# Optimization experiments

Measured on AMD Instinct MI355X. Metric: run time of the kernel, lower is better.

## Reference

```python
import jax, jax.numpy as jnp
import numpy as np

C = 128      # block channels
K = 7        # involution kernel size
GC = 16      # group_ch
G = (C // 2) // GC  # involution groups = 4


def conv1x1(x, w, b):
    # x: (B,Cin,H,W), w: (Cout,Cin)
    return jnp.einsum('bchw,oc->bohw', x, w) + b[None, :, None, None]


def conv2d(x, w, b, pad):
    y = jax.lax.conv_general_dilated(
        x, w, window_strides=(1, 1), padding=((pad, pad), (pad, pad)),
        dimension_numbers=('NCHW', 'OIHW', 'NCHW'))
    return y + b[None, :, None, None]


def prelu(x, a):
    return jnp.where(x >= 0, x, a * x)


def patches7(x):
    # x: (B,C,H,W) -> (B,C,K*K,H,W), same padding (torch Unfold, pad=3)
    B, Cc, H, W = x.shape
    p = K // 2
    xp = jnp.pad(x, ((0, 0), (0, 0), (p, p), (p, p)))
    return jnp.stack([xp[:, :, i:i + H, j:j + W]
                      for i in range(K) for j in range(K)], axis=2)


def setup_inputs() -> dict:
    key = jax.random.key(0)
    ks = jax.random.split(key, 9)
    f32 = jnp.float32
    def w(k, shape, s=0.02):
        return jax.random.normal(k, shape, f32) * s
    d = {}
    d['x'] = jax.random.normal(ks[0], (2, C, 128, 128), f32)
    # conv1: C -> C//2, 1x1
    d['w1'] = w(ks[1], (C // 2, C)); d['b1'] = jnp.zeros((C // 2,), f32)
    d['a1'] = jnp.float32(0.25)  # PReLU (single param)
    # involution reduce: C//2 -> C//4, 1x1 (+ReLU)
    d['wr'] = w(ks[2], (C // 4, C // 2)); d['br'] = jnp.zeros((C // 4,), f32)
    # involution span: C//4 -> G*K*K, 1x1
    d['ws'] = w(ks[3], (G * K * K, C // 4)); d['bs'] = jnp.zeros((G * K * K,), f32)
    d['a2'] = jnp.float32(0.25)
    # conv2: C//2 -> C, 1x1
    d['w2'] = w(ks[4], (C, C // 2)); d['b2'] = jnp.zeros((C,), f32)
    # attn conv: 2 -> 1, 7x7 pad 3
    d['wa'] = w(ks[5], (1, 2, 7, 7)); d['ba'] = jnp.zeros((1,), f32)
    # psec: 3x3 (C//4->C//4) + PReLU + 1x1 (C//4->C)
    d['wp1'] = w(ks[6], (C // 4, C // 4, 3, 3)); d['bp1'] = jnp.zeros((C // 4,), f32)
    d['ap'] = jnp.float32(0.25)
    d['wp2'] = w(ks[7], (C, C // 4)); d['bp2'] = jnp.zeros((C,), f32)
    return d


def reference(x, w1, b1, a1, wr, br, ws, bs, a2, w2, b2, wa, ba, wp1, bp1, ap, wp2, bp2):
    B, _, H, W = x.shape
    x1 = prelu(conv1x1(x, w1, b1), a1)                       # (B, C/2, H, W)
    # involution: per-pixel dynamic kernels
    f = jax.nn.relu(conv1x1(x1, wr, br))                     # (B, C/4, H, W)
    kw = conv1x1(f, ws, bs).reshape(B, G, 1, K * K, H, W)    # dynamic kernels
    pat = patches7(x1).reshape(B, G, GC, K * K, H, W)        # unfolded patches
    x2 = (kw * pat).sum(axis=3).reshape(B, C // 2, H, W)     # multiply-reduce
    x3 = conv1x1(prelu(x2, a2), w2, b2)                      # (B, C, H, W)
    # attention gate on f (ZPool -> 7x7 conv -> sigmoid)
    zp = jnp.concatenate([f.max(axis=1, keepdims=True),
                          f.mean(axis=1, keepdims=True)], axis=1)
    attn = jax.nn.sigmoid(conv2d(zp, wa, ba, 3))             # (B, 1, H, W)
    x4 = x3 * attn
    ps = conv1x1(prelu(conv2d(f, wp1, bp1, 1), ap), wp2, bp2)
    return x4 + ps
```

## Files before the change

### kernel.cpp

```cpp
#include <hip/hip_runtime.h>

#define HW_  16384
#define NPX  32768

__device__ __forceinline__ float prelu_(float x, float a) { return x >= 0.f ? x : a * x; }

__global__ __launch_bounds__(256, 2) void k_front(const float* __restrict__ x,
        const float* __restrict__ w1, const float* __restrict__ b1,
        const float* __restrict__ a1p, const float* __restrict__ wr,
        const float* __restrict__ br, float* __restrict__ x1,
        float* __restrict__ f, float* __restrict__ zp) {
    __shared__ float sA[12352];
    float* xs  = sA;
    float* wT1 = sA + 4096;
    int p0 = blockIdx.x << 6;
    int b = p0 >> 14, hw0 = p0 & 16383;

    for (int e = threadIdx.x; e < 8192; e += 256) {
        int o = e >> 7, c = e & 127;
        wT1[o * 129 + c] = w1[e];
    }
    int pq = threadIdx.x & 15;
    int og = threadIdx.x >> 4;
    const float a1 = a1p[0];
    float4 acc[4];
    #pragma unroll
    for (int u = 0; u < 4; ++u) { float bv = b1[og * 4 + u]; acc[u] = make_float4(bv, bv, bv, bv); }
    const float* xb = x + (b << 21) + hw0;
    #pragma unroll 1
    for (int half = 0; half < 2; ++half) {
        float4 xv[4];
        #pragma unroll
        for (int i = 0; i < 4; ++i) {
            int e = threadIdx.x + (i << 8);
            xv[i] = *(const float4*)&xb[((half * 64 + (e >> 4)) << 14) + ((e & 15) << 2)];
        }
        __syncthreads();
        #pragma unroll
        for (int i = 0; i < 4; ++i) {
            int e = threadIdx.x + (i << 8);
            *(float4*)&xs[((e >> 4) << 6) + ((e & 15) << 2)] = xv[i];
        }
        __syncthreads();
        #pragma unroll 4
        for (int c2 = 0; c2 < 64; ++c2) {
            float4 tap = *(const float4*)&xs[(c2 << 6) + (pq << 2)];
            int c = (half << 6) + c2;
            #pragma unroll
            for (int u = 0; u < 4; ++u) {
                float wv = wT1[(og * 4 + u) * 129 + c];
                acc[u].x = fmaf(wv, tap.x, acc[u].x);
                acc[u].y = fmaf(wv, tap.y, acc[u].y);
                acc[u].z = fmaf(wv, tap.z, acc[u].z);
                acc[u].w = fmaf(wv, tap.w, acc[u].w);
            }
        }
    }
    float4 res[4];
    #pragma unroll
    for (int u = 0; u < 4; ++u) {
        res[u].x = prelu_(acc[u].x, a1); res[u].y = prelu_(acc[u].y, a1);
        res[u].z = prelu_(acc[u].z, a1); res[u].w = prelu_(acc[u].w, a1);
        *(float4*)(x1 + ((b * 64 + og * 4 + u) << 14) + hw0 + (pq << 2)) = res[u];
    }
    __syncthreads();
    float* x1t = sA;
    float* wrT = sA + 4352;
    float* ft  = sA + 6432;
    #pragma unroll
    for (int u = 0; u < 4; ++u)
        *(float4*)&x1t[(og * 4 + u) * 68 + (pq << 2)] = res[u];
    for (int e = threadIdx.x; e < 2048; e += 256) {
        int fo = e >> 6, c = e & 63;
        wrT[fo * 65 + c] = wr[e];
    }
    __syncthreads();
    int pq2 = threadIdx.x & 15;
    int fg = threadIdx.x >> 4;
    float4 fa[2];
    #pragma unroll
    for (int u = 0; u < 2; ++u) { float bv = br[fg * 2 + u]; fa[u] = make_float4(bv, bv, bv, bv); }
    #pragma unroll 4
    for (int c = 0; c < 64; ++c) {
        float4 tap = *(const float4*)&x1t[c * 68 + (pq2 << 2)];
        #pragma unroll
        for (int u = 0; u < 2; ++u) {
            float wv = wrT[(fg * 2 + u) * 65 + c];
            fa[u].x = fmaf(wv, tap.x, fa[u].x);
            fa[u].y = fmaf(wv, tap.y, fa[u].y);
            fa[u].z = fmaf(wv, tap.z, fa[u].z);
            fa[u].w = fmaf(wv, tap.w, fa[u].w);
        }
    }
    #pragma unroll
    for (int u = 0; u < 2; ++u) {
        float4 r;
        r.x = fmaxf(fa[u].x, 0.f); r.y = fmaxf(fa[u].y, 0.f);
        r.z = fmaxf(fa[u].z, 0.f); r.w = fmaxf(fa[u].w, 0.f);
        *(float4*)(f + ((b * 32 + fg * 2 + u) << 14) + hw0 + (pq2 << 2)) = r;
        *(float4*)&ft[(fg * 2 + u) * 68 + (pq2 << 2)] = r;
    }
    __syncthreads();
    if (threadIdx.x < 64) {
        int px = threadIdx.x;
        float mx = ft[px], sm = ft[px];
        #pragma unroll
        for (int c = 1; c < 32; ++c) {
            float v = ft[c * 68 + px];
            mx = fmaxf(mx, v); sm += v;
        }
        zp[((b * 2 + 0) << 14) + hw0 + px] = mx;
        zp[((b * 2 + 1) << 14) + hw0 + px] = sm * (1.f / 32.f);
    }
}

__global__ __launch_bounds__(256) void k_mid2(const float* __restrict__ x1,
        const float* __restrict__ f, const float* __restrict__ ws_,
        const float* __restrict__ bs, float* __restrict__ x2,
        const float* __restrict__ zp, const float* __restrict__ wp1,
        const float* __restrict__ bp1, const float* __restrict__ app,
        float* __restrict__ p1, const float* __restrict__ wa,
        const float* __restrict__ ba, float* __restrict__ attn) {
    __shared__ float smem[10688];
    if (blockIdx.x < 512) {
        float* tile = smem;
        int g = blockIdx.x >> 7;
        int t = blockIdx.x & 127;
        int b = t >> 6;
        int th = (t >> 3) & 7, tw = t & 7;
        int h0 = th * 16, w0 = tw * 16;
        const float* x1g = x1 + ((b * 64 + g * 16) << 14);
        #pragma unroll 1
        for (int rem = threadIdx.x; rem < 484; rem += 256) {
            int r = rem / 22, cl = rem - r * 22;
            int hh = h0 + r - 3, ww = w0 + cl - 3;
            bool ok = (hh >= 0 && hh < 128 && ww >= 0 && ww < 128);
            const float* src = x1g + (hh << 7) + ww;
            float v[16];
            #pragma unroll
            for (int c = 0; c < 16; ++c) v[c] = ok ? src[c << 14] : 0.f;
            float* dst = tile + r * 24 + cl;
            #pragma unroll
            for (int c = 0; c < 16; ++c) dst[c * 528] = v[c];
        }
        int lh = threadIdx.x >> 4, lw = threadIdx.x & 15;
        int hw = ((h0 + lh) << 7) + w0 + lw;
        float fv[32];
        const float* fp = f + (b << 19) + hw;
        #pragma unroll
        for (int c = 0; c < 32; ++c) fv[c] = fp[c << 14];
        __syncthreads();
        float acc[16];
        #pragma unroll
        for (int u = 0; u < 16; ++u) acc[u] = 0.f;
        const float* tap0 = tile + lh * 24 + lw;
        const float* wk = ws_ + g * 49 * 32;
        const float* bsg = bs + g * 49;
        #pragma unroll 1
        for (int di = 0; di < 7; ++di) {
            #pragma unroll 1
            for (int dj = 0; dj < 7; ++dj) {
                int kk = di * 7 + dj;
                float kwv = bsg[kk];
                const float* wkk = wk + kk * 32;
                #pragma unroll
                for (int c = 0; c < 32; ++c) kwv = fmaf(wkk[c], fv[c], kwv);
                const float* tp = tap0 + di * 24 + dj;
                #pragma unroll
                for (int u = 0; u < 16; ++u)
                    acc[u] = fmaf(kwv, tp[u * 528], acc[u]);
            }
        }
        float* op = x2 + ((b * 64 + g * 16) << 14) + hw;
        #pragma unroll
        for (int u = 0; u < 16; ++u) op[u << 14] = acc[u];
    } else if (blockIdx.x < 1024) {
        float* fs = smem;
        float* wT = smem + 6080;
        int bid = blockIdx.x - 512;
        int half = bid >> 8;
        int t = bid & 255;
        int b = t >> 7;
        int tl = t & 127;
        int th = tl >> 3, tw = tl & 7;
        int h0 = th * 8, w0 = tw * 16;
        int o0 = half * 16;
        const float4* wsrc4 = (const float4*)(wp1 + o0 * 288);
        #pragma unroll 1
        for (int e4 = threadIdx.x; e4 < 1152; e4 += 256) {
            float4 v = wsrc4[e4];
            int o = e4 / 72, r4 = (e4 - o * 72) * 4;
            wT[(r4 + 0) * 16 + o] = v.x;
            wT[(r4 + 1) * 16 + o] = v.y;
            wT[(r4 + 2) * 16 + o] = v.z;
            wT[(r4 + 3) * 16 + o] = v.w;
        }
        const float* fb = f + (b << 19);
        #pragma unroll 1
        for (int rem = threadIdx.x; rem < 180; rem += 256) {
            int r = rem / 18, cl = rem - r * 18;
            int hh = h0 + r - 1, ww = w0 + cl - 1;
            bool ok = (hh >= 0 && hh < 128 && ww >= 0 && ww < 128);
            const float* src = fb + (hh << 7) + ww;
            float* dst = fs + r * 19 + cl;
            #pragma unroll 1
            for (int cb = 0; cb < 4; ++cb) {
                float v[8];
                #pragma unroll
                for (int c = 0; c < 8; ++c) v[c] = ok ? src[(cb * 8 + c) << 14] : 0.f;
                #pragma unroll
                for (int c = 0; c < 8; ++c) dst[(cb * 8 + c) * 190] = v[c];
            }
        }
        __syncthreads();
        int pxq = threadIdx.x & 31;
        int rowq = pxq >> 2, colq = pxq & 3;
        int oh = threadIdx.x >> 5;
        const float ap = app[0];
        float acc[2][4];
        #pragma unroll
        for (int o = 0; o < 2; ++o) {
            float bv = bp1[o0 + oh * 2 + o];
            #pragma unroll
            for (int px = 0; px < 4; ++px) acc[o][px] = bv;
        }
        const float* fsb = fs + rowq * 19 + colq * 4;
        for (int ci = 0; ci < 32; ++ci) {
            float tap[3][6];
            const float* base = fsb + ci * 190;
            #pragma unroll
            for (int r = 0; r < 3; ++r)
                #pragma unroll
                for (int j = 0; j < 6; ++j)
                    tap[r][j] = base[r * 19 + j];
            #pragma unroll
            for (int ki = 0; ki < 3; ++ki)
                #pragma unroll
                for (int kj = 0; kj < 3; ++kj) {
                    float2 wv = *(const float2*)&wT[((ci * 9 + ki * 3 + kj) << 4) + oh * 2];
                    #pragma unroll
                    for (int px = 0; px < 4; ++px) {
                        float tv = tap[ki][px + kj];
                        acc[0][px] = fmaf(wv.x, tv, acc[0][px]);
                        acc[1][px] = fmaf(wv.y, tv, acc[1][px]);
                    }
                }
        }
        int hw = ((h0 + rowq) << 7) + w0 + colq * 4;
        #pragma unroll
        for (int o = 0; o < 2; ++o) {
            float4 r;
            r.x = prelu_(acc[o][0], ap); r.y = prelu_(acc[o][1], ap);
            r.z = prelu_(acc[o][2], ap); r.w = prelu_(acc[o][3], ap);
            *(float4*)(p1 + ((b * 32 + o0 + oh * 2 + o) << 14) + hw) = r;
        }
    } else {
        float* zs = smem;
        int t = blockIdx.x - 1024;
        int b = t >> 6;
        int tile = t & 63;
        int th = tile >> 3, tw = tile & 7;
        int h0 = th * 16, w0 = tw * 16;
        const float* zb = zp + (b << 15);
        #pragma unroll 1
        for (int rem = threadIdx.x; rem < 484; rem += 256) {
            int r = rem / 22, cl = rem - r * 22;
            int hh = h0 + r - 3, ww = w0 + cl - 3;
            bool ok = (hh >= 0 && hh < 128 && ww >= 0 && ww < 128);
            const float* src = zb + (hh << 7) + ww;
            float v0 = ok ? src[0] : 0.f;
            float v1 = ok ? src[HW_] : 0.f;
            zs[r * 23 + cl] = v0;
            zs[506 + r * 23 + cl] = v1;
        }
        __syncthreads();
        int lh = threadIdx.x >> 4, lw = threadIdx.x & 15;
        float acc = ba[0];
        #pragma unroll
        for (int c = 0; c < 2; ++c) {
            const float* zc = &zs[c * 506 + lh * 23 + lw];
            #pragma unroll
            for (int i = 0; i < 7; ++i)
                #pragma unroll
                for (int j = 0; j < 7; ++j)
                    acc = fmaf(wa[c * 49 + i * 7 + j], zc[i * 23 + j], acc);
        }
        attn[(b << 14) + ((h0 + lh) << 7) + w0 + lw] = 1.f / (1.f + expf(-acc));
    }
}

__global__ __launch_bounds__(256, 2) void k_final(const float* __restrict__ x2,
        const float* __restrict__ p1, const float* __restrict__ attn,
        const float* __restrict__ a2p, const float* __restrict__ w2,
        const float* __restrict__ b2, const float* __restrict__ wp2,
        const float* __restrict__ bp2, float* __restrict__ out) {
    __shared__ float xs2[64 * 128];
    __shared__ float ps[32 * 128];
    __shared__ float wT2[64 * 36];
    __shared__ float wTp[32 * 36];
    __shared__ float as_[128];
    int split = blockIdx.x >> 8;
    int tile = blockIdx.x & 255;
    int b = tile >> 7;
    int hw0 = (tile & 127) << 7;
    int o0 = split * 32;
    const float a2 = a2p[0];

    for (int e = threadIdx.x; e < 2048; e += 256) {
        int o = e >> 6, c = e & 63;
        wT2[c * 36 + o] = w2[(o0 + o) * 64 + c];
    }
    for (int e = threadIdx.x; e < 1024; e += 256) {
        int o = e >> 5, c = e & 31;
        wTp[c * 36 + o] = wp2[(o0 + o) * 32 + c];
    }
    {
        const float4* xb = (const float4*)(x2 + (b << 20) + hw0);
        float4 xv[8];
        #pragma unroll
        for (int i = 0; i < 8; ++i) {
            int e = threadIdx.x + i * 256;
            xv[i] = xb[((e >> 5) << 12) + (e & 31)];
        }
        #pragma unroll
        for (int i = 0; i < 8; ++i) {
            int e = threadIdx.x + i * 256;
            float4 v = xv[i];
            v.x = prelu_(v.x, a2); v.y = prelu_(v.y, a2);
            v.z = prelu_(v.z, a2); v.w = prelu_(v.w, a2);
            *(float4*)&xs2[(e >> 5) * 128 + (e & 31) * 4] = v;
        }
        const float4* pb = (const float4*)(p1 + (b << 19) + hw0);
        float4 pv[4];
        #pragma unroll
        for (int i = 0; i < 4; ++i) {
            int e = threadIdx.x + i * 256;
            pv[i] = pb[((e >> 5) << 12) + (e & 31)];
        }
        #pragma unroll
        for (int i = 0; i < 4; ++i) {
            int e = threadIdx.x + i * 256;
            *(float4*)&ps[(e >> 5) * 128 + (e & 31) * 4] = pv[i];
        }
        if (threadIdx.x < 32)
            ((float4*)as_)[threadIdx.x] = ((const float4*)(attn + (b << 14) + hw0))[threadIdx.x];
    }
    int pr = threadIdx.x & 63;
    int og = threadIdx.x >> 6;
    float b2v[8], bpv[8];
    #pragma unroll
    for (int u = 0; u < 8; ++u) { b2v[u] = b2[o0 + og * 8 + u]; bpv[u] = bp2[o0 + og * 8 + u]; }
    __syncthreads();

    float2 acc[8];
    #pragma unroll
    for (int u = 0; u < 8; ++u) acc[u] = make_float2(0.f, 0.f);
    #pragma unroll 8
    for (int c = 0; c < 64; ++c) {
        float2 tap = *(const float2*)&xs2[c * 128 + pr * 2];
        const float* wb = &wT2[c * 36 + og * 8];
        float4 wva = *(const float4*)wb;
        float4 wvb = *(const float4*)(wb + 4);
        acc[0].x = fmaf(wva.x, tap.x, acc[0].x); acc[0].y = fmaf(wva.x, tap.y, acc[0].y);
        acc[1].x = fmaf(wva.y, tap.x, acc[1].x); acc[1].y = fmaf(wva.y, tap.y, acc[1].y);
        acc[2].x = fmaf(wva.z, tap.x, acc[2].x); acc[2].y = fmaf(wva.z, tap.y, acc[2].y);
        acc[3].x = fmaf(wva.w, tap.x, acc[3].x); acc[3].y = fmaf(wva.w, tap.y, acc[3].y);
        acc[4].x = fmaf(wvb.x, tap.x, acc[4].x); acc[4].y = fmaf(wvb.x, tap.y, acc[4].y);
        acc[5].x = fmaf(wvb.y, tap.x, acc[5].x); acc[5].y = fmaf(wvb.y, tap.y, acc[5].y);
        acc[6].x = fmaf(wvb.z, tap.x, acc[6].x); acc[6].y = fmaf(wvb.z, tap.y, acc[6].y);
        acc[7].x = fmaf(wvb.w, tap.x, acc[7].x); acc[7].y = fmaf(wvb.w, tap.y, acc[7].y);
    }
    float2 at = *(const float2*)&as_[pr * 2];
    #pragma unroll
    for (int u = 0; u < 8; ++u) {
        acc[u].x = (acc[u].x + b2v[u]) * at.x + bpv[u];
        acc[u].y = (acc[u].y + b2v[u]) * at.y + bpv[u];
    }
    #pragma unroll 8
    for (int c = 0; c < 32; ++c) {
        float2 tap = *(const float2*)&ps[c * 128 + pr * 2];
        const float* wb = &wTp[c * 36 + og * 8];
        float4 wva = *(const float4*)wb;
        float4 wvb = *(const float4*)(wb + 4);
        acc[0].x = fmaf(wva.x, tap.x, acc[0].x); acc[0].y = fmaf(wva.x, tap.y, acc[0].y);
        acc[1].x = fmaf(wva.y, tap.x, acc[1].x); acc[1].y = fmaf(wva.y, tap.y, acc[1].y);
        acc[2].x = fmaf(wva.z, tap.x, acc[2].x); acc[2].y = fmaf(wva.z, tap.y, acc[2].y);
        acc[3].x = fmaf(wva.w, tap.x, acc[3].x); acc[3].y = fmaf(wva.w, tap.y, acc[3].y);
        acc[4].x = fmaf(wvb.x, tap.x, acc[4].x); acc[4].y = fmaf(wvb.x, tap.y, acc[4].y);
        acc[5].x = fmaf(wvb.y, tap.x, acc[5].x); acc[5].y = fmaf(wvb.y, tap.y, acc[5].y);
        acc[6].x = fmaf(wvb.z, tap.x, acc[6].x); acc[6].y = fmaf(wvb.z, tap.y, acc[6].y);
        acc[7].x = fmaf(wvb.w, tap.x, acc[7].x); acc[7].y = fmaf(wvb.w, tap.y, acc[7].y);
    }
    #pragma unroll
    for (int u = 0; u < 8; ++u)
        *(float2*)(out + ((b * 128 + o0 + og * 8 + u) << 14) + hw0 + pr * 2) = acc[u];
}

extern "C" void kernel_launch(void* const* d_in, const int* in_sizes, int n_in,
                              void* d_out, int out_size, void* d_ws, size_t ws_size,
                              hipStream_t stream) {
    const float* x   = (const float*)d_in[0];
    const float* w1  = (const float*)d_in[1];
    const float* b1  = (const float*)d_in[2];
    const float* a1  = (const float*)d_in[3];
    const float* wr  = (const float*)d_in[4];
    const float* br  = (const float*)d_in[5];
    const float* ws_ = (const float*)d_in[6];
    const float* bs  = (const float*)d_in[7];
    const float* a2  = (const float*)d_in[8];
    const float* w2  = (const float*)d_in[9];
    const float* b2  = (const float*)d_in[10];
    const float* wa  = (const float*)d_in[11];
    const float* ba  = (const float*)d_in[12];
    const float* wp1 = (const float*)d_in[13];
    const float* bp1 = (const float*)d_in[14];
    const float* ap  = (const float*)d_in[15];
    const float* wp2 = (const float*)d_in[16];
    const float* bp2 = (const float*)d_in[17];
    float* out = (float*)d_out;

    float* w = (float*)d_ws;
    float* ws_x1   = w;
    float* ws_f    = ws_x1 + 2 * 64 * HW_;
    float* ws_x2   = ws_f  + 2 * 32 * HW_;
    float* ws_zp   = ws_x2 + 2 * 64 * HW_;
    float* ws_attn = ws_zp + 2 * 2 * HW_;
    float* ws_p1   = ws_attn + NPX;

    hipLaunchKernelGGL(k_front, dim3(512), dim3(256), 0, stream,
                       x, w1, b1, a1, wr, br, ws_x1, ws_f, ws_zp);
    hipLaunchKernelGGL(k_mid2, dim3(1152), dim3(256), 0, stream,
                       ws_x1, ws_f, ws_, bs, ws_x2, ws_zp,
                       wp1, bp1, ap, ws_p1, wa, ba, ws_attn);
    hipLaunchKernelGGL(k_final, dim3(1024), dim3(256), 0, stream,
                       ws_x2, ws_p1, ws_attn, a2, w2, b2, wp2, bp2, out);
}
```

Measured before the change: 182.8 us.

## Vectorize front-conv weight reads and halve mid-kernel shared memory for occupancy

In k_front, the 1x1 conv weights are now read as float4 with a 132-float row pad, and four channel taps are loaded per iteration, so the LDS instruction count per FMA drops. The launch bound rises to 3 blocks per SM. In k_mid2, the 3x3 conv weights are staged in two halves of 16 input channels each, so shared memory shrinks from 10688 to 8448 floats and the launch bound can be raised to 4 blocks. In exchange, the 3x3 path gets extra barriers and non-coalesced weight reloads, and the higher occupancy targets may force register spills.

```diff
diff --git a/kernel.cpp b/kernel.cpp
--- a/kernel.cpp
+++ b/kernel.cpp
@@ -5,12 +5,12 @@
 
 __device__ __forceinline__ float prelu_(float x, float a) { return x >= 0.f ? x : a * x; }
 
-__global__ __launch_bounds__(256, 2) void k_front(const float* __restrict__ x,
+__global__ __launch_bounds__(256, 3) void k_front(const float* __restrict__ x,
         const float* __restrict__ w1, const float* __restrict__ b1,
         const float* __restrict__ a1p, const float* __restrict__ wr,
         const float* __restrict__ br, float* __restrict__ x1,
         float* __restrict__ f, float* __restrict__ zp) {
-    __shared__ float sA[12352];
+    __shared__ float sA[12544];
     float* xs  = sA;
     float* wT1 = sA + 4096;
     int p0 = blockIdx.x << 6;
@@ -18,7 +18,7 @@
 
     for (int e = threadIdx.x; e < 8192; e += 256) {
         int o = e >> 7, c = e & 127;
-        wT1[o * 129 + c] = w1[e];
+        wT1[o * 132 + c] = w1[e];
     }
     int pq = threadIdx.x & 15;
     int og = threadIdx.x >> 4;
@@ -43,16 +43,22 @@
         }
         __syncthreads();
         #pragma unroll 4
-        for (int c2 = 0; c2 < 64; ++c2) {
-            float4 tap = *(const float4*)&xs[(c2 << 6) + (pq << 2)];
-            int c = (half << 6) + c2;
+        for (int c4 = 0; c4 < 16; ++c4) {
+            float4 taps[4];
+            #pragma unroll
+            for (int j = 0; j < 4; ++j)
+                taps[j] = *(const float4*)&xs[((c4 * 4 + j) << 6) + (pq << 2)];
             #pragma unroll
             for (int u = 0; u < 4; ++u) {
-                float wv = wT1[(og * 4 + u) * 129 + c];
-                acc[u].x = fmaf(wv, tap.x, acc[u].x);
-                acc[u].y = fmaf(wv, tap.y, acc[u].y);
-                acc[u].z = fmaf(wv, tap.z, acc[u].z);
-                acc[u].w = fmaf(wv, tap.w, acc[u].w);
+                float4 wv = *(const float4*)&wT1[(og * 4 + u) * 132 + half * 64 + c4 * 4];
+                acc[u].x = fmaf(wv.x, taps[0].x, acc[u].x); acc[u].y = fmaf(wv.x, taps[0].y, acc[u].y);
+                acc[u].z = fmaf(wv.x, taps[0].z, acc[u].z); acc[u].w = fmaf(wv.x, taps[0].w, acc[u].w);
+                acc[u].x = fmaf(wv.y, taps[1].x, acc[u].x); acc[u].y = fmaf(wv.y, taps[1].y, acc[u].y);
+                acc[u].z = fmaf(wv.y, taps[1].z, acc[u].z); acc[u].w = fmaf(wv.y, taps[1].w, acc[u].w);
+                acc[u].x = fmaf(wv.z, taps[2].x, acc[u].x); acc[u].y = fmaf(wv.z, taps[2].y, acc[u].y);
+                acc[u].z = fmaf(wv.z, taps[2].z, acc[u].z); acc[u].w = fmaf(wv.z, taps[2].w, acc[u].w);
+                acc[u].x = fmaf(wv.w, taps[3].x, acc[u].x); acc[u].y = fmaf(wv.w, taps[3].y, acc[u].y);
+                acc[u].z = fmaf(wv.w, taps[3].z, acc[u].z); acc[u].w = fmaf(wv.w, taps[3].w, acc[u].w);
             }
         }
     }
@@ -114,14 +120,14 @@
     }
 }
 
-__global__ __launch_bounds__(256) void k_mid2(const float* __restrict__ x1,
+__global__ __launch_bounds__(256, 4) void k_mid2(const float* __restrict__ x1,
         const float* __restrict__ f, const float* __restrict__ ws_,
         const float* __restrict__ bs, float* __restrict__ x2,
         const float* __restrict__ zp, const float* __restrict__ wp1,
         const float* __restrict__ bp1, const float* __restrict__ app,
         float* __restrict__ p1, const float* __restrict__ wa,
         const float* __restrict__ ba, float* __restrict__ attn) {
-    __shared__ float smem[10688];
+    __shared__ float smem[8448];
     if (blockIdx.x < 512) {
         float* tile = smem;
         int g = blockIdx.x >> 7;
@@ -185,16 +191,6 @@
         int th = tl >> 3, tw = tl & 7;
         int h0 = th * 8, w0 = tw * 16;
         int o0 = half * 16;
-        const float4* wsrc4 = (const float4*)(wp1 + o0 * 288);
-        #pragma unroll 1
-        for (int e4 = threadIdx.x; e4 < 1152; e4 += 256) {
-            float4 v = wsrc4[e4];
-            int o = e4 / 72, r4 = (e4 - o * 72) * 4;
-            wT[(r4 + 0) * 16 + o] = v.x;
-            wT[(r4 + 1) * 16 + o] = v.y;
-            wT[(r4 + 2) * 16 + o] = v.z;
-            wT[(r4 + 3) * 16 + o] = v.w;
-        }
         const float* fb = f + (b << 19);
         #pragma unroll 1
         for (int rem = threadIdx.x; rem < 180; rem += 256) {
@@ -212,7 +208,6 @@
                 for (int c = 0; c < 8; ++c) dst[(cb * 8 + c) * 190] = v[c];
             }
         }
-        __syncthreads();
         int pxq = threadIdx.x & 31;
         int rowq = pxq >> 2, colq = pxq & 3;
         int oh = threadIdx.x >> 5;
@@ -225,26 +220,40 @@
             for (int px = 0; px < 4; ++px) acc[o][px] = bv;
         }
         const float* fsb = fs + rowq * 19 + colq * 4;
-        for (int ci = 0; ci < 32; ++ci) {
-            float tap[3][6];
-            const float* base = fsb + ci * 190;
-            #pragma unroll
-            for (int r = 0; r < 3; ++r)
-                #pragma unroll
-                for (int j = 0; j < 6; ++j)
-                    tap[r][j] = base[r * 19 + j];
-            #pragma unroll
-            for (int ki = 0; ki < 3; ++ki)
-                #pragma unroll
-                for (int kj = 0; kj < 3; ++kj) {
-                    float2 wv = *(const float2*)&wT[((ci * 9 + ki * 3 + kj) << 4) + oh * 2];
+        #pragma unroll 1
+        for (int cih = 0; cih < 2; ++cih) {
+            __syncthreads();
+            #pragma unroll 1
+            for (int e = threadIdx.x; e < 2304; e += 256) {
+                int o = e / 144, i = e - o * 144;
+                wT[o * 145 + i] = wp1[(o0 + o) * 288 + cih * 144 + i];
+            }
+            __syncthreads();
+            #pragma unroll 1
+            for (int cl_ = 0; cl_ < 16; ++cl_) {
+                int ci = cih * 16 + cl_;
+                float tap[3][6];
+                const float* base = fsb + ci * 190;
+                #pragma unroll
+                for (int r = 0; r < 3; ++r)
                     #pragma unroll
-                    for (int px = 0; px < 4; ++px) {
-                        float tv = tap[ki][px + kj];
-                        acc[0][px] = fmaf(wv.x, tv, acc[0][px]);
-                        acc[1][px] = fmaf(wv.y, tv, acc[1][px]);
+                    for (int j = 0; j < 6; ++j)
+                        tap[r][j] = base[r * 19 + j];
+                #pragma unroll
+                for (int ki = 0; ki < 3; ++ki)
+                    #pragma unroll
+                    for (int kj = 0; kj < 3; ++kj) {
+                        int idx = cl_ * 9 + ki * 3 + kj;
+                        float w0v = wT[(oh * 2 + 0) * 145 + idx];
+                        float w1v = wT[(oh * 2 + 1) * 145 + idx];
+                        #pragma unroll
+                        for (int px = 0; px < 4; ++px) {
+                            float tv = tap[ki][px + kj];
+                            acc[0][px] = fmaf(w0v, tv, acc[0][px]);
+                            acc[1][px] = fmaf(w1v, tv, acc[1][px]);
+                        }
                     }
-                }
+            }
         }
         int hw = ((h0 + rowq) << 7) + w0 + colq * 4;
         #pragma unroll
```

Measured after the change: 176.3 us. 3.5% less time.
